# Kernel optimization log

Measured on AMD Instinct MI355X. Metric: run time of the kernel, lower is better.

## Reference

```python
import jax, jax.numpy as jnp
import numpy as np

N, G, C, H, S = 16384, 100, 10, 32, 10  # batch, nb_genes, nb_chrom, hidden, signature
BN_EPS = 1e-5
SLOPE = 0.2


def setup_inputs() -> dict:
    key = jax.random.key(0)
    k = jax.random.split(key, 7)
    x = jax.random.randint(k[0], (N, G), 0, 3)                      # categorical genotype per gene
    emb = jax.random.normal(k[1], (G, 3, H), dtype=jnp.float32)      # per-gene entity embedding tables
    gene_att = jax.random.normal(k[2], (C, H), dtype=jnp.float32)    # GeneAttentionLayer attention matrix
    chrom_att = jax.random.normal(k[3], (1, H), dtype=jnp.float32)   # ChromAttentionLayer attention vector
    W = jax.random.normal(k[4], (H, S), dtype=jnp.float32) * 0.1     # linear layer weight
    b = jnp.zeros((S,), dtype=jnp.float32)                           # linear layer bias
    bn_gamma = jnp.ones((S,), dtype=jnp.float32)
    bn_beta = jnp.zeros((S,), dtype=jnp.float32)
    return {"x": x, "emb": emb, "gene_att": gene_att, "chrom_att": chrom_att,
            "W": W, "b": b, "bn_gamma": bn_gamma, "bn_beta": bn_beta}


def reference(x, emb, gene_att, chrom_att, W, b, bn_gamma, bn_beta):
    nb_genes, nb_chrom, hid = emb.shape[0], gene_att.shape[0], emb.shape[2]
    genes_per_chrom = nb_genes // nb_chrom
    # chrom composition matrix: comp[i, j] = 1 iff gene j belongs to chromosome i (contiguous blocks)
    comp = (jnp.arange(nb_genes) // genes_per_chrom == jnp.arange(nb_chrom)[:, None]).astype(emb.dtype)

    # --- entity embedding: h[n, g] = emb[g, x[n, g]]  -> (N, G, H)
    h = emb[jnp.arange(nb_genes)[None, :], x]

    # --- GeneAttentionLayer (avoids the dense (N, C, G, H) intermediate of the torch code)
    att = jnp.einsum('ch,ngh->ncg', gene_att, h) * comp[None]        # (N, C, G)
    mask = (att != 0).astype(h.dtype)                                # matches att.bool().byte()
    a = jnp.exp(jax.nn.leaky_relu(att, SLOPE)) * mask
    a = a / jnp.maximum(a.sum(axis=2, keepdims=True), 1e-10)
    chrom = jnp.einsum('ncg,ngh->nch', a, h)                         # (N, C, H) chromosome embeddings
    chrom = jax.nn.relu(chrom)                                       # dropout p=0 -> identity

    # --- ChromAttentionLayer
    catt = jnp.einsum('h,nch->nc', chrom_att[0], chrom)              # (N, C)
    ca = jnp.exp(jax.nn.leaky_relu(catt, SLOPE))
    ca = ca / ca.sum(axis=1, keepdims=True)
    g = jnp.einsum('nc,nch->nh', ca, chrom)                          # (N, H)
    g = jax.nn.relu(g)

    # --- linear + batch norm (training-mode batch statistics, biased variance as in torch BN)
    y = g @ W + b                                                    # (N, S)
    mu = y.mean(axis=0)
    var = ((y - mu) ** 2).mean(axis=0)
    return (y - mu) / jnp.sqrt(var + BN_EPS) * bn_gamma + bn_beta
```

## Files before the change

kernel.cpp:

```cpp
#include <hip/hip_runtime.h>
#include <hip/hip_fp16.h>

#define NROWS 16384
#define NG 100
#define NC 10
#define NH 32
#define NS 10
#define GPC 10
#define SLOPE 0.2f
#define BN_EPS 1e-5f

#define RPB 32
#define BLOCK_A 512
#define NB (NROWS / RPB)

template<int CTRL>
__device__ __forceinline__ float dpp_add(float v) {
    int x = __builtin_bit_cast(int, v);
    int y = __builtin_amdgcn_update_dpp(0, x, CTRL, 0xF, 0xF, true);
    return v + __builtin_bit_cast(float, y);
}
__device__ __forceinline__ float row16_allreduce(float v) {
    v = dpp_add<0x128>(v);
    v = dpp_add<0x124>(v);
    v = dpp_add<0x122>(v);
    v = dpp_add<0x121>(v);
    return v;
}
__device__ __forceinline__ float uniform16_wavesum_lane63(float v) {
    v = dpp_add<0x142>(v);
    v = dpp_add<0x143>(v);
    return v;
}

#define GATHER(c, arr, pkv)                                                \
    _Pragma("unroll")                                                      \
    for (int gp = 0; gp < GPC; ++gp) {                                     \
        const int g_ = (c) * GPC + gp;                                     \
        const unsigned xg_ = (pkv[g_ >> 4] >> ((g_ & 15) * 2)) & 3u;       \
        const int r3_ = g_ * 3 + (int)xg_;                                 \
        arr[gp] = cmbL[r3_ * 16 + o];                                      \
    }

#define COMPUTE(arr, num, den) do {                                        \
    float e_[GPC];                                                         \
    _Pragma("unroll")                                                      \
    for (int gp = 0; gp < GPC; ++gp)                                       \
        e_[gp] = __builtin_bit_cast(float, arr[gp].y);                     \
    const float s01_ = (e_[0] + e_[1]) + (e_[2] + e_[3]);                  \
    const float s23_ = (e_[4] + e_[5]) + (e_[6] + e_[7]);                  \
    const float suma_ = (s01_ + s23_) + (e_[8] + e_[9]);                   \
    const float inv_ = 1.f / fmaxf(suma_, 1e-10f);                         \
    float2 chA_ = {0.f, 0.f}, chB_ = {0.f, 0.f};                           \
    _Pragma("unroll")                                                      \
    for (int gp = 0; gp < GPC; gp += 2) {                                  \
        float2 h0_ = __half22float2(__builtin_bit_cast(__half2, arr[gp].x)); \
        float2 h1_ = __half22float2(__builtin_bit_cast(__half2, arr[gp+1].x)); \
        chA_.x = fmaf(e_[gp],   h0_.x, chA_.x);                            \
        chA_.y = fmaf(e_[gp],   h0_.y, chA_.y);                            \
        chB_.x = fmaf(e_[gp+1], h1_.x, chB_.x);                            \
        chB_.y = fmaf(e_[gp+1], h1_.y, chB_.y);                            \
    }                                                                      \
    float2 ch_ = {chA_.x + chB_.x, chA_.y + chB_.y};                       \
    ch_.x = fmaxf(ch_.x, 0.f);    \
    ch_.y = fmaxf(ch_.y, 0.f);                                             \
    float pc_ = ch_.x * ca.x + ch_.y * ca.y;                               \
    pc_ = row16_allreduce(pc_);                                            \
    pc_ *= inv_;                                           \
    const float lc_ = pc_ > 0.f ? pc_ : SLOPE * pc_;                       \
    const float ec_ = __expf(lc_);                                         \
    const float w_ = ec_ * inv_;                                           \
    num.x = fmaf(w_, ch_.x, num.x);                                        \
    num.y = fmaf(w_, ch_.y, num.y);                                        \
    den += ec_;                                                            \
} while (0)

template<bool SLOTS>
__global__ __launch_bounds__(BLOCK_A, 4) void gga_main(
    const int* __restrict__ x, const float* __restrict__ emb,
    const float* __restrict__ gene_att, const float* __restrict__ chrom_att,
    const float* __restrict__ W, const float* __restrict__ b,
    float* __restrict__ y, float* __restrict__ P)
{
    __shared__ uint2 cmbL[300 * 16];
    __shared__ float eL[300];
    __shared__ float WTL[NS * NH];
    __shared__ float bL[NS];
    __shared__ unsigned xpL[RPB * 8];
    __shared__ float sAcc[2 * NS];

    const int t = threadIdx.x;
    const int n0 = blockIdx.x * RPB;

    const int pr = t >> 3, pw = t & 7;
    int4 xv0, xv1, xv2, xv3;
    if (t < 256 && pw < 7) {
        const int4* p = reinterpret_cast<const int4*>(x + (n0 + pr) * NG + pw * 16);
        xv0 = p[0];
        if (pw < 6) { xv1 = p[1]; xv2 = p[2]; xv3 = p[3]; }
    }
    unsigned hreg[10];
#pragma unroll
    for (int i2 = 0; i2 < 10; ++i2) {
        const int i = t + i2 * BLOCK_A;
        if (i < 4800) {
            float2 hv = reinterpret_cast<const float2*>(emb)[i];
            hreg[i2] = __builtin_bit_cast(unsigned, __floats2half2_rn(hv.x, hv.y));
        }
    }
    if (t < 300) {
        const int g = t / 3;
        const float* ga = gene_att + (g / GPC) * NH;
        const float* e = emb + t * NH;
        float s = 0.f;
#pragma unroll
        for (int k = 0; k < NH; k += 4) {
            float4 ev = *reinterpret_cast<const float4*>(e + k);
            float4 gv = *reinterpret_cast<const float4*>(ga + k);
            s = fmaf(gv.x, ev.x, s); s = fmaf(gv.y, ev.y, s);
            s = fmaf(gv.z, ev.z, s); s = fmaf(gv.w, ev.w, s);
        }
        const float lk = s > 0.f ? s : SLOPE * s;
        eL[t] = (s != 0.f) ? __expf(lk) : 0.f;
    }
    if (t < 256) {
        unsigned pwv = 0u;
        if (pw < 7) {
            const int nv = (pw < 6) ? 4 : 1;
            int4 vv[4] = {xv0, xv1, xv2, xv3};
#pragma unroll
            for (int i = 0; i < 4; ++i) {
                if (i < nv) {
                    pwv |= ((unsigned)vv[i].x & 3u) << (i * 8 + 0);
                    pwv |= ((unsigned)vv[i].y & 3u) << (i * 8 + 2);
                    pwv |= ((unsigned)vv[i].z & 3u) << (i * 8 + 4);
                    pwv |= ((unsigned)vv[i].w & 3u) << (i * 8 + 6);
                }
            }
        }
        xpL[pr * 8 + pw] = pwv;
    }
    if (t < NH * NS) WTL[t] = W[(t & 31) * NS + (t >> 5)];
    if (t < NS) bL[t] = b[t];
    if (t < 2 * NS) sAcc[t] = 0.f;
    __syncthreads();

#pragma unroll
    for (int i2 = 0; i2 < 10; ++i2) {
        const int i = t + i2 * BLOCK_A;
        if (i < 4800) {
            uint2 en;
            en.x = hreg[i2];
            en.y = __builtin_bit_cast(unsigned, eL[i >> 4]);
            cmbL[i] = en;
        }
    }
    __syncthreads();

    const int lr = t >> 4;
    const int o = t & 15;
    const int n = n0 + lr;

    const float2 ca = reinterpret_cast<const float2*>(chrom_att)[o];

    const uint4 pa = *reinterpret_cast<const uint4*>(&xpL[lr * 8]);
    const uint4 pb = *reinterpret_cast<const uint4*>(&xpL[lr * 8 + 4]);
    const unsigned pk[8] = {pa.x, pa.y, pa.z, pa.w, pb.x, pb.y, pb.z, pb.w};

    float2 num = {0.f, 0.f};
    float den = 0.f;

    uint2 hA[GPC], hB[GPC];
    GATHER(0, hA, pk);
#pragma unroll
    for (int c = 0; c < NC; ++c) {
        if ((c & 1) == 0) { if (c + 1 < NC) { GATHER(c + 1, hB, pk); } COMPUTE(hA, num, den); }
        else              { if (c + 1 < NC) { GATHER(c + 1, hA, pk); } COMPUTE(hB, num, den); }
    }

    const float invd = 1.f / den;
    const float g0 = fmaxf(num.x * invd, 0.f);
    const float g1 = fmaxf(num.y * invd, 0.f);

    float ys[NS];
#pragma unroll
    for (int s = 0; s < NS; ++s) {
        const float2 wv = *reinterpret_cast<const float2*>(&WTL[s * NH + o * 2]);
        float p = g0 * wv.x + g1 * wv.y;
        p = row16_allreduce(p);
        ys[s] = p + bL[s];
    }

    if (o == 0) {
        float2* yp = reinterpret_cast<float2*>(y + n * NS);
#pragma unroll
        for (int s2 = 0; s2 < 5; ++s2) yp[s2] = make_float2(ys[2 * s2], ys[2 * s2 + 1]);
    }

#pragma unroll
    for (int s = 0; s < NS; ++s) {
        float v  = uniform16_wavesum_lane63(ys[s]);
        float v2 = uniform16_wavesum_lane63(ys[s] * ys[s]);
        if ((t & 63) == 63) { atomicAdd(&sAcc[s], v); atomicAdd(&sAcc[NS + s], v2); }
    }
    __syncthreads();
    if (t < 2 * NS) {
        if (SLOTS) P[t * NB + blockIdx.x] = sAcc[t];
        else       atomicAdd(&P[t], sAcc[t]);
    }
}

template<bool SLOTS>
__global__ __launch_bounds__(512) void gga_bn(
    float* __restrict__ out, const float* __restrict__ P,
    const float* __restrict__ gamma, const float* __restrict__ beta)
{
    __shared__ float red[2 * NS * 8];
    __shared__ float scL[NS], shL[NS];
    const int t = threadIdx.x;

    if (SLOTS) {
        if (t < 2 * NS * 8) {
            const int k = t >> 3, c = t & 7;
            const float4* p4 = reinterpret_cast<const float4*>(P + k * NB + c * 64);
            float s = 0.f;
#pragma unroll
            for (int i = 0; i < 16; ++i) {
                float4 v = p4[i];
                s += v.x + v.y + v.z + v.w;
            }
            red[t] = s;
        }
        __syncthreads();
    }
    if (t < NS) {
        float sm, sq;
        if (SLOTS) {
            sm = 0.f; sq = 0.f;
#pragma unroll
            for (int c = 0; c < 8; ++c) {
                sm += red[t * 8 + c];
                sq += red[(NS + t) * 8 + c];
            }
        } else {
            sm = P[t]; sq = P[NS + t];
        }
        const float mu = sm * (1.f / NROWS);
        float var = sq * (1.f / NROWS) - mu * mu;
        var = fmaxf(var, 0.f);
        const float r = rsqrtf(var + BN_EPS);
        scL[t] = gamma[t] * r;
        shL[t] = beta[t] - mu * scL[t];
    }
    __syncthreads();

    const int i4 = (blockIdx.x * 512 + t) * 4;
    float4 v = *reinterpret_cast<const float4*>(out + i4);
    const int s0 = i4 % NS;
    const int s1 = (s0 + 1) % NS, s2 = (s0 + 2) % NS, s3 = (s0 + 3) % NS;
    v.x = fmaf(v.x, scL[s0], shL[s0]);
    v.y = fmaf(v.y, scL[s1], shL[s1]);
    v.z = fmaf(v.z, scL[s2], shL[s2]);
    v.w = fmaf(v.w, scL[s3], shL[s3]);
    *reinterpret_cast<float4*>(out + i4) = v;
}

extern "C" void kernel_launch(void* const* d_in, const int* in_sizes, int n_in,
                              void* d_out, int out_size, void* d_ws, size_t ws_size,
                              hipStream_t stream) {
    const int*   x         = (const int*)d_in[0];
    const float* emb       = (const float*)d_in[1];
    const float* gene_att  = (const float*)d_in[2];
    const float* chrom_att = (const float*)d_in[3];
    const float* W         = (const float*)d_in[4];
    const float* b         = (const float*)d_in[5];
    const float* bn_gamma  = (const float*)d_in[6];
    const float* bn_beta   = (const float*)d_in[7];

    float* y = (float*)d_out;
    float* P = (float*)d_ws;

    if (ws_size >= (size_t)(2 * NS * NB * sizeof(float))) {
        gga_main<true><<<NB, BLOCK_A, 0, stream>>>(
            x, emb, gene_att, chrom_att, W, b, y, P);
        gga_bn<true><<<(NROWS * NS) / (512 * 4), 512, 0, stream>>>(
            y, P, bn_gamma, bn_beta);
    } else {
        hipMemsetAsync(P, 0, 2 * NS * sizeof(float), stream);
        gga_main<false><<<NB, BLOCK_A, 0, stream>>>(
            x, emb, gene_att, chrom_att, W, b, y, P);
        gga_bn<false><<<(NROWS * NS) / (512 * 4), 512, 0, stream>>>(
            y, P, bn_gamma, bn_beta);
    }
}
```

Measured before the change: 24.67 us.

## Double rows per block, drop register prefetch of emb, shrink BN blocks

The main kernel now handles 64 rows per 1024-thread block. This halves the number of blocks that each redo the 300-entry emb/attention table setup in shared memory, so the per-block setup is amortised over twice as many rows. The emb-to-half conversion no longer stages values in registers across the first barrier; it loads directly in the fill loop, and the x packing is done by the first 512 threads. The BN kernel uses 256-thread blocks and a smaller partial-sum reduction sized to the halved block count. The trade-off is larger blocks with launch_bounds(1024,4), which may limit occupancy, and the emb loads are no longer overlapped with the x and attention setup.

```diff
diff --git a/kernel.cpp b/kernel.cpp
--- a/kernel.cpp
+++ b/kernel.cpp
@@ -10,8 +10,8 @@
 #define SLOPE 0.2f
 #define BN_EPS 1e-5f
 
-#define RPB 32
-#define BLOCK_A 512
+#define RPB 64
+#define BLOCK_A 1024
 #define NB (NROWS / RPB)
 
 template<int CTRL>
@@ -92,22 +92,6 @@
     const int t = threadIdx.x;
     const int n0 = blockIdx.x * RPB;
 
-    const int pr = t >> 3, pw = t & 7;
-    int4 xv0, xv1, xv2, xv3;
-    if (t < 256 && pw < 7) {
-        const int4* p = reinterpret_cast<const int4*>(x + (n0 + pr) * NG + pw * 16);
-        xv0 = p[0];
-        if (pw < 6) { xv1 = p[1]; xv2 = p[2]; xv3 = p[3]; }
-    }
-    unsigned hreg[10];
-#pragma unroll
-    for (int i2 = 0; i2 < 10; ++i2) {
-        const int i = t + i2 * BLOCK_A;
-        if (i < 4800) {
-            float2 hv = reinterpret_cast<const float2*>(emb)[i];
-            hreg[i2] = __builtin_bit_cast(unsigned, __floats2half2_rn(hv.x, hv.y));
-        }
-    }
     if (t < 300) {
         const int g = t / 3;
         const float* ga = gene_att + (g / GPC) * NH;
@@ -123,34 +107,38 @@
         const float lk = s > 0.f ? s : SLOPE * s;
         eL[t] = (s != 0.f) ? __expf(lk) : 0.f;
     }
-    if (t < 256) {
-        unsigned pwv = 0u;
-        if (pw < 7) {
-            const int nv = (pw < 6) ? 4 : 1;
-            int4 vv[4] = {xv0, xv1, xv2, xv3};
-#pragma unroll
-            for (int i = 0; i < 4; ++i) {
-                if (i < nv) {
-                    pwv |= ((unsigned)vv[i].x & 3u) << (i * 8 + 0);
-                    pwv |= ((unsigned)vv[i].y & 3u) << (i * 8 + 2);
-                    pwv |= ((unsigned)vv[i].z & 3u) << (i * 8 + 4);
-                    pwv |= ((unsigned)vv[i].w & 3u) << (i * 8 + 6);
-                }
-            }
-        }
-        xpL[pr * 8 + pw] = pwv;
-    }
     if (t < NH * NS) WTL[t] = W[(t & 31) * NS + (t >> 5)];
     if (t < NS) bL[t] = b[t];
     if (t < 2 * NS) sAcc[t] = 0.f;
-    __syncthreads();
-
-#pragma unroll
-    for (int i2 = 0; i2 < 10; ++i2) {
+    if (t < 512) {
+        const int r = t >> 3, w = t & 7;
+        unsigned pw = 0u;
+        if (w < 7) {
+            const int4* p = reinterpret_cast<const int4*>(x + (n0 + r) * NG + w * 16);
+            const int nv = (w < 6) ? 4 : 1;
+#pragma unroll
+            for (int i = 0; i < 4; ++i) {
+                if (i < nv) {
+                    int4 v = p[i];
+                    pw |= ((unsigned)v.x & 3u) << (i * 8 + 0);
+                    pw |= ((unsigned)v.y & 3u) << (i * 8 + 2);
+                    pw |= ((unsigned)v.z & 3u) << (i * 8 + 4);
+                    pw |= ((unsigned)v.w & 3u) << (i * 8 + 6);
+                }
+            }
+        }
+        xpL[r * 8 + w] = pw;
+    }
+    __syncthreads();
+
+#pragma unroll
+    for (int i2 = 0; i2 < 5; ++i2) {
         const int i = t + i2 * BLOCK_A;
         if (i < 4800) {
+            float2 hv = reinterpret_cast<const float2*>(emb)[i];
+            __half2 h2 = __floats2half2_rn(hv.x, hv.y);
             uint2 en;
-            en.x = hreg[i2];
+            en.x = __builtin_bit_cast(unsigned, h2);
             en.y = __builtin_bit_cast(unsigned, eL[i >> 4]);
             cmbL[i] = en;
         }
@@ -211,7 +199,7 @@
 }
 
 template<bool SLOTS>
-__global__ __launch_bounds__(512) void gga_bn(
+__global__ __launch_bounds__(256) void gga_bn(
     float* __restrict__ out, const float* __restrict__ P,
     const float* __restrict__ gamma, const float* __restrict__ beta)
 {
@@ -222,10 +210,10 @@
     if (SLOTS) {
         if (t < 2 * NS * 8) {
             const int k = t >> 3, c = t & 7;
-            const float4* p4 = reinterpret_cast<const float4*>(P + k * NB + c * 64);
+            const float4* p4 = reinterpret_cast<const float4*>(P + k * NB + c * 32);
             float s = 0.f;
 #pragma unroll
-            for (int i = 0; i < 16; ++i) {
+            for (int i = 0; i < 8; ++i) {
                 float4 v = p4[i];
                 s += v.x + v.y + v.z + v.w;
             }
@@ -254,7 +242,7 @@
     }
     __syncthreads();
 
-    const int i4 = (blockIdx.x * 512 + t) * 4;
+    const int i4 = (blockIdx.x * 256 + t) * 4;
     float4 v = *reinterpret_cast<const float4*>(out + i4);
     const int s0 = i4 % NS;
     const int s1 = (s0 + 1) % NS, s2 = (s0 + 2) % NS, s3 = (s0 + 3) % NS;
@@ -283,13 +271,13 @@
     if (ws_size >= (size_t)(2 * NS * NB * sizeof(float))) {
         gga_main<true><<<NB, BLOCK_A, 0, stream>>>(
             x, emb, gene_att, chrom_att, W, b, y, P);
-        gga_bn<true><<<(NROWS * NS) / (512 * 4), 512, 0, stream>>>(
+        gga_bn<true><<<(NROWS * NS) / (256 * 4), 256, 0, stream>>>(
             y, P, bn_gamma, bn_beta);
     } else {
         hipMemsetAsync(P, 0, 2 * NS * sizeof(float), stream);
         gga_main<false><<<NB, BLOCK_A, 0, stream>>>(
             x, emb, gene_att, chrom_att, W, b, y, P);
-        gga_bn<false><<<(NROWS * NS) / (512 * 4), 512, 0, stream>>>(
+        gga_bn<false><<<(NROWS * NS) / (256 * 4), 256, 0, stream>>>(
             y, P, bn_gamma, bn_beta);
     }
 }
```

New measurement: 22.67 us. 8.1% less time.
